# Optimization experiments

Hardware: AMD Instinct MI355X
Metric: run time of the kernel (lower is better)

## Reference

```python
import jax, jax.numpy as jnp
import numpy as np

DIM = 192
HEADS = 6
WH, WW = 8, 8
N = WH * WW
B_ = 2048
NW = 512


def _relative_position_index():
    coords = np.stack(np.meshgrid(np.arange(WH), np.arange(WW), indexing='ij'))  # 2,Wh,Ww
    cf = coords.reshape(2, -1)
    rel = cf[:, :, None] - cf[:, None, :]  # 2,N,N
    rel = rel.transpose(1, 2, 0).astype(np.int32)
    rel[:, :, 0] += WH - 1
    rel[:, :, 1] += WW - 1
    rel[:, :, 0] *= 2 * WW - 1
    return jnp.asarray(rel.sum(-1))  # N,N int32


def setup_inputs() -> dict:
    key = jax.random.key(0)
    ks = jax.random.split(key, 16)
    s = 0.02
    inp = {
        'q': jax.random.normal(ks[0], (B_, N, DIM), jnp.float32),
        'k': jax.random.normal(ks[1], (B_, N, DIM), jnp.float32),
        'v': jax.random.normal(ks[2], (B_, N, DIM), jnp.float32),
        'mask': jax.random.normal(ks[3], (NW, N, N), jnp.float32),
        'attn_mask': jax.random.randint(ks[4], (B_, 1, N, N), 0, 2).astype(bool),
        'Wq': jax.random.normal(ks[5], (DIM, DIM), jnp.float32) * s,
        'bq': jnp.zeros((DIM,), jnp.float32),
        'Wk': jax.random.normal(ks[6], (DIM, DIM), jnp.float32) * s,
        'bk': jnp.zeros((DIM,), jnp.float32),
        'Wv': jax.random.normal(ks[7], (DIM, DIM), jnp.float32) * s,
        'bv': jnp.zeros((DIM,), jnp.float32),
        'Wp': jax.random.normal(ks[8], (DIM, DIM), jnp.float32) * s,
        'bp': jnp.zeros((DIM,), jnp.float32),
        'rpb_table': jax.random.normal(ks[9], ((2 * WH - 1) * (2 * WW - 1), HEADS), jnp.float32) * s,
        'rel_idx': _relative_position_index(),
    }
    return inp


def reference(q, k, v, mask, attn_mask, Wq, bq, Wk, bk, Wv, bv, Wp, bp, rpb_table, rel_idx):
    Bw, n, C = q.shape
    hd = C // HEADS
    scale = hd ** (-0.5)
    # linear projections (torch Linear: x @ W.T + b), split heads -> b h n d
    qh = (q @ Wq.T + bq).reshape(Bw, n, HEADS, hd).transpose(0, 2, 1, 3) * scale
    kh = (k @ Wk.T + bk).reshape(Bw, n, HEADS, hd).transpose(0, 2, 1, 3)
    vh = (v @ Wv.T + bv).reshape(Bw, n, HEADS, hd).transpose(0, 2, 1, 3)
    attn = jnp.einsum('bhnd,bhmd->bhnm', qh, kh)  # (B_, H, N, N)
    attn = jnp.where(attn_mask, jnp.float32(-1e9), attn)
    # relative position bias gather: (N,N,H) -> (H,N,N)
    bias = rpb_table[rel_idx.reshape(-1)].reshape(n, n, HEADS).transpose(2, 0, 1)
    attn = attn + bias[None]
    nW = mask.shape[0]
    attn = attn.reshape(Bw // nW, nW, HEADS, n, n) + mask[None, :, None]
    attn = jax.nn.softmax(attn.reshape(Bw, HEADS, n, n), axis=-1)
    x = jnp.einsum('bhnm,bhmd->bhnd', attn, vh).transpose(0, 2, 1, 3).reshape(Bw, n, C)
    return x @ Wp.T + bp
```

## Files before the change

### kernel.cpp

```cpp
#include <hip/hip_runtime.h>

#define DIM    192
#define HEADS  6
#define HD     32
#define NTOK   64
#define NWIN   512
#define NBLK   2048
#define TPB    384
#define XPITCH 200
#define MPITCH 65

typedef short  bf16x4 __attribute__((ext_vector_type(4)));
typedef short  bf16x8 __attribute__((ext_vector_type(8)));
typedef float  f32x4  __attribute__((ext_vector_type(4)));

#if defined(__HIP_DEVICE_COMPILE__)
#if !__has_builtin(__builtin_amdgcn_mfma_f32_16x16x32_bf16)
#error "missing __builtin_amdgcn_mfma_f32_16x16x32_bf16"
#endif
#if !__has_builtin(__builtin_amdgcn_mfma_f32_16x16x16bf16_1k)
#error "missing __builtin_amdgcn_mfma_f32_16x16x16bf16_1k"
#endif
#endif

static __device__ __forceinline__ unsigned short f2bf(float f){
  unsigned u = __builtin_bit_cast(unsigned, f);
  u += 0x7FFFu + ((u >> 16) & 1u);
  return (unsigned short)(u >> 16);
}

static __device__ __forceinline__ f32x4 mfma32(bf16x8 a, bf16x8 b, f32x4 c){
  return __builtin_amdgcn_mfma_f32_16x16x32_bf16(a, b, c, 0, 0, 0);
}
static __device__ __forceinline__ f32x4 mfma16(bf16x4 a, bf16x4 b, f32x4 c){
  return __builtin_amdgcn_mfma_f32_16x16x16bf16_1k(a, b, c, 0, 0, 0);
}

static __device__ __forceinline__ bf16x8 load_wfrag(const float* __restrict__ W, int row, int k0){
  const float4 a = *(const float4*)(W + row*DIM + k0);
  const float4 b = *(const float4*)(W + row*DIM + k0 + 4);
  bf16x8 r;
  r[0]=(short)f2bf(a.x); r[1]=(short)f2bf(a.y); r[2]=(short)f2bf(a.z); r[3]=(short)f2bf(a.w);
  r[4]=(short)f2bf(b.x); r[5]=(short)f2bf(b.y); r[6]=(short)f2bf(b.z); r[7]=(short)f2bf(b.w);
  return r;
}

static __device__ __forceinline__ void stage_xin(unsigned short* xin, const float* __restrict__ src, int t){
  #pragma unroll
  for (int j = 0; j < 8; ++j){
    const int i4  = t + j*TPB;
    const float4 f = ((const float4*)src)[i4];
    const int row = i4 / 48;
    const int col = (i4 - row*48) * 4;
    uint2 u;
    u.x = (unsigned)f2bf(f.x) | ((unsigned)f2bf(f.y) << 16);
    u.y = (unsigned)f2bf(f.z) | ((unsigned)f2bf(f.w) << 16);
    *(uint2*)(xin + row*XPITCH + col) = u;
  }
}

__global__ void detect_amask_kernel(const unsigned int* __restrict__ am, int* __restrict__ mode){
  __shared__ int sawFloat, sawByte;
  if (threadIdx.x == 0){ sawFloat = 0; sawByte = 0; }
  __syncthreads();
  const uint4 ld = ((const uint4*)am)[threadIdx.x];
  unsigned w[4] = {ld.x, ld.y, ld.z, ld.w};
  int f = 0, bm = 0;
  #pragma unroll
  for (int i = 0; i < 4; ++i){
    if (w[i] == 0x3F800000u) f = 1;
    else if (w[i] & ~1u)     bm = 1;
  }
  if (f)  atomicOr(&sawFloat, 1);
  if (bm) atomicOr(&sawByte, 1);
  __syncthreads();
  if (threadIdx.x == 0) *mode = sawFloat ? 2 : (sawByte ? 1 : 0);
}

__global__ void bias_pre_kernel(const float* __restrict__ rpb, const int* __restrict__ rel_idx,
                                float* __restrict__ bias_pre){
  const int e = blockIdx.x*256 + threadIdx.x;
  if (e >= HEADS*NTOK*NTOK) return;
  const int rest = e & 4095, m = rest >> 6, n = rest & 63;
  bias_pre[e] = rpb[rel_idx[n*NTOK + m]*HEADS + (e >> 12)];
}

__global__ __launch_bounds__(TPB, 2) void swin_kernel(
  const float* __restrict__ q, const float* __restrict__ kin, const float* __restrict__ vin,
  const float* __restrict__ mask, const void* __restrict__ amask,
  const float* __restrict__ Wq, const float* __restrict__ bq,
  const float* __restrict__ Wk, const float* __restrict__ bk,
  const float* __restrict__ Wv, const float* __restrict__ bv,
  const float* __restrict__ Wp, const float* __restrict__ bp,
  const float* __restrict__ bias_pre, const int* __restrict__ mflag,
  float* __restrict__ out)
{
  __shared__ unsigned short xin[NTOK * XPITCH];
  __shared__ float madd[NTOK * MPITCH];

  const int b    = blockIdx.x;
  const int t    = threadIdx.x;
  const int h    = t >> 6;
  const int lane = t & 63;
  const int l15  = lane & 15;
  const int g    = lane >> 4;
  const int c0   = h * HD;
  const size_t base = (size_t)b * (NTOK * DIM);
  const float scale = 0.17677669529663687f;
  const f32x4 fz = {0.f, 0.f, 0.f, 0.f};

  {
    const int mode = mflag[0];
    const float* mrow = mask + (size_t)(b & (NWIN-1)) * (NTOK*NTOK);
    const size_t abase = (size_t)b * (NTOK*NTOK);
    for (int i = t; i < NTOK*NTOK; i += TPB){
      const int n = i >> 6, m = i & 63;
      bool msk;
      if (mode == 0)      msk = ((const int*)amask)[abase + i] != 0;
      else if (mode == 1) msk = ((const unsigned char*)amask)[abase + i] != 0;
      else                msk = ((const float*)amask)[abase + i] != 0.0f;
      madd[m*MPITCH + n] = mrow[i] + (msk ? -1e9f : 0.0f);
    }
    stage_xin(xin, q + base, t);
  }
  __syncthreads();

  bf16x4 Qf[4][2], Kf[4][2], Vf[2][4];

  {
    f32x4 acc[2][4];
    #pragma unroll
    for (int a0=0;a0<2;++a0){
      #pragma unroll
      for (int a1=0;a1<4;++a1) acc[a0][a1] = fz;
    }
    #pragma unroll
    for (int kt = 0; kt < 6; ++kt){
      const int k0 = kt*32 + g*8;
      const bf16x8 w0 = load_wfrag(Wq, c0 + l15, k0);
      const bf16x8 w1 = load_wfrag(Wq, c0 + 16 + l15, k0);
      #pragma unroll
      for (int nt = 0; nt < 4; ++nt){
        const bf16x8 xf = *(const bf16x8*)(xin + (nt*16 + l15)*XPITCH + k0);
        acc[0][nt] = mfma32(w0, xf, acc[0][nt]);
        acc[1][nt] = mfma32(w1, xf, acc[1][nt]);
      }
    }
    #pragma unroll
    for (int dt = 0; dt < 2; ++dt){
      const float4 bb = *(const float4*)(bq + c0 + dt*16 + g*4);
      #pragma unroll
      for (int nt = 0; nt < 4; ++nt){
        bf16x4 f;
        f[0]=(short)f2bf((acc[dt][nt][0]+bb.x)*scale);
        f[1]=(short)f2bf((acc[dt][nt][1]+bb.y)*scale);
        f[2]=(short)f2bf((acc[dt][nt][2]+bb.z)*scale);
        f[3]=(short)f2bf((acc[dt][nt][3]+bb.w)*scale);
        Qf[nt][dt] = f;
      }
    }
  }
  __syncthreads();
  stage_xin(xin, kin + base, t);
  __syncthreads();

  {
    f32x4 acc[2][4];
    #pragma unroll
    for (int a0=0;a0<2;++a0){
      #pragma unroll
      for (int a1=0;a1<4;++a1) acc[a0][a1] = fz;
    }
    #pragma unroll
    for (int kt = 0; kt < 6; ++kt){
      const int k0 = kt*32 + g*8;
      const bf16x8 w0 = load_wfrag(Wk, c0 + l15, k0);
      const bf16x8 w1 = load_wfrag(Wk, c0 + 16 + l15, k0);
      #pragma unroll
      for (int mt = 0; mt < 4; ++mt){
        const bf16x8 xf = *(const bf16x8*)(xin + (mt*16 + l15)*XPITCH + k0);
        acc[0][mt] = mfma32(w0, xf, acc[0][mt]);
        acc[1][mt] = mfma32(w1, xf, acc[1][mt]);
      }
    }
    #pragma unroll
    for (int dt = 0; dt < 2; ++dt){
      const float4 bb = *(const float4*)(bk + c0 + dt*16 + g*4);
      #pragma unroll
      for (int mt = 0; mt < 4; ++mt){
        bf16x4 f;
        f[0]=(short)f2bf(acc[dt][mt][0]+bb.x);
        f[1]=(short)f2bf(acc[dt][mt][1]+bb.y);
        f[2]=(short)f2bf(acc[dt][mt][2]+bb.z);
        f[3]=(short)f2bf(acc[dt][mt][3]+bb.w);
        Kf[mt][dt] = f;
      }
    }
  }
  __syncthreads();
  stage_xin(xin, vin + base, t);
  __syncthreads();

  {
    f32x4 acc[4][2];
    #pragma unroll
    for (int a0=0;a0<4;++a0){
      #pragma unroll
      for (int a1=0;a1<2;++a1) acc[a0][a1] = fz;
    }
    #pragma unroll
    for (int kt = 0; kt < 6; ++kt){
      const int k0 = kt*32 + g*8;
      const bf16x8 w0 = load_wfrag(Wv, c0 + l15, k0);
      const bf16x8 w1 = load_wfrag(Wv, c0 + 16 + l15, k0);
      #pragma unroll
      for (int mt = 0; mt < 4; ++mt){
        const bf16x8 xf = *(const bf16x8*)(xin + (mt*16 + l15)*XPITCH + k0);
        acc[mt][0] = mfma32(xf, w0, acc[mt][0]);
        acc[mt][1] = mfma32(xf, w1, acc[mt][1]);
      }
    }
    const float bv0 = bv[c0 + l15];
    const float bv1 = bv[c0 + 16 + l15];
    #pragma unroll
    for (int mt = 0; mt < 4; ++mt){
      bf16x4 f0, f1;
      f0[0]=(short)f2bf(acc[mt][0][0]+bv0); f0[1]=(short)f2bf(acc[mt][0][1]+bv0);
      f0[2]=(short)f2bf(acc[mt][0][2]+bv0); f0[3]=(short)f2bf(acc[mt][0][3]+bv0);
      f1[0]=(short)f2bf(acc[mt][1][0]+bv1); f1[1]=(short)f2bf(acc[mt][1][1]+bv1);
      f1[2]=(short)f2bf(acc[mt][1][2]+bv1); f1[3]=(short)f2bf(acc[mt][1][3]+bv1);
      Vf[0][mt] = f0;
      Vf[1][mt] = f1;
    }
  }
  __syncthreads();

  f32x4 s[4][4];
  #pragma unroll
  for (int mt = 0; mt < 4; ++mt){
    #pragma unroll
    for (int nt = 0; nt < 4; ++nt){
      f32x4 a = mfma16(Kf[mt][0], Qf[nt][0], fz);
      s[mt][nt] = mfma16(Kf[mt][1], Qf[nt][1], a);
    }
  }

  const float* bh = bias_pre + h * (NTOK*NTOK);
  bf16x4 Pf[4][4];
  #pragma unroll
  for (int nt = 0; nt < 4; ++nt){
    const int n = nt*16 + l15;
    float mx = -3.0e38f;
    #pragma unroll
    for (int mt = 0; mt < 4; ++mt){
      #pragma unroll
      for (int r = 0; r < 4; ++r){
        const int m = mt*16 + g*4 + r;
        const float val = s[mt][nt][r] + madd[m*MPITCH + n] + bh[m*64 + n];
        s[mt][nt][r] = val;
        mx = fmaxf(mx, val);
      }
    }
    mx = fmaxf(mx, __shfl_xor(mx, 16, 64));
    mx = fmaxf(mx, __shfl_xor(mx, 32, 64));
    float sum = 0.f;
    #pragma unroll
    for (int mt = 0; mt < 4; ++mt){
      #pragma unroll
      for (int r = 0; r < 4; ++r){
        const float e = __expf(s[mt][nt][r] - mx);
        s[mt][nt][r] = e;
        sum += e;
      }
    }
    sum += __shfl_xor(sum, 16, 64);
    sum += __shfl_xor(sum, 32, 64);
    const float inv = 1.0f / sum;
    #pragma unroll
    for (int ms = 0; ms < 4; ++ms){
      bf16x4 f;
      f[0]=(short)f2bf(s[ms][nt][0]*inv); f[1]=(short)f2bf(s[ms][nt][1]*inv);
      f[2]=(short)f2bf(s[ms][nt][2]*inv); f[3]=(short)f2bf(s[ms][nt][3]*inv);
      Pf[nt][ms] = f;
    }
  }

  f32x4 o[2][4];
  #pragma unroll
  for (int a0=0;a0<2;++a0){
    #pragma unroll
    for (int a1=0;a1<4;++a1) o[a0][a1] = fz;
  }
  #pragma unroll
  for (int ms = 0; ms < 4; ++ms){
    #pragma unroll
    for (int dt = 0; dt < 2; ++dt){
      #pragma unroll
      for (int nt = 0; nt < 4; ++nt){
        o[dt][nt] = mfma16(Vf[dt][ms], Pf[nt][ms], o[dt][nt]);
      }
    }
  }

  #pragma unroll
  for (int dt = 0; dt < 2; ++dt){
    #pragma unroll
    for (int nt = 0; nt < 4; ++nt){
      const int n   = nt*16 + l15;
      const int col = c0 + dt*16 + g*4;
      uint2 u;
      u.x = (unsigned)f2bf(o[dt][nt][0]) | ((unsigned)f2bf(o[dt][nt][1]) << 16);
      u.y = (unsigned)f2bf(o[dt][nt][2]) | ((unsigned)f2bf(o[dt][nt][3]) << 16);
      *(uint2*)(xin + n*XPITCH + col) = u;
    }
  }
  __syncthreads();

  {
    f32x4 acc[4][2];
    #pragma unroll
    for (int a0=0;a0<4;++a0){
      #pragma unroll
      for (int a1=0;a1<2;++a1) acc[a0][a1] = fz;
    }
    #pragma unroll
    for (int kt = 0; kt < 6; ++kt){
      const int k0 = kt*32 + g*8;
      const bf16x8 w0 = load_wfrag(Wp, c0 + l15, k0);
      const bf16x8 w1 = load_wfrag(Wp, c0 + 16 + l15, k0);
      #pragma unroll
      for (int nt = 0; nt < 4; ++nt){
        const bf16x8 xf = *(const bf16x8*)(xin + (nt*16 + l15)*XPITCH + k0);
        acc[nt][0] = mfma32(xf, w0, acc[nt][0]);
        acc[nt][1] = mfma32(xf, w1, acc[nt][1]);
      }
    }
    const float bp0 = bp[c0 + l15];
    const float bp1 = bp[c0 + 16 + l15];
    #pragma unroll
    for (int nt = 0; nt < 4; ++nt){
      #pragma unroll
      for (int ctl = 0; ctl < 2; ++ctl){
        const int c = c0 + ctl*16 + l15;
        const float badd = ctl ? bp1 : bp0;
        #pragma unroll
        for (int r = 0; r < 4; ++r){
          const int n = nt*16 + g*4 + r;
          out[base + (size_t)(n*DIM + c)] = acc[nt][ctl][r] + badd;
        }
      }
    }
  }
}

extern "C" void kernel_launch(void* const* d_in, const int* in_sizes, int n_in,
                              void* d_out, int out_size, void* d_ws, size_t ws_size,
                              hipStream_t stream){
  const float* q     = (const float*)d_in[0];
  const float* k     = (const float*)d_in[1];
  const float* v     = (const float*)d_in[2];
  const float* mask  = (const float*)d_in[3];
  const void*  amask = d_in[4];
  const float* Wq    = (const float*)d_in[5];
  const float* bq    = (const float*)d_in[6];
  const float* Wk    = (const float*)d_in[7];
  const float* bk    = (const float*)d_in[8];
  const float* Wv    = (const float*)d_in[9];
  const float* bv    = (const float*)d_in[10];
  const float* Wp    = (const float*)d_in[11];
  const float* bp    = (const float*)d_in[12];
  const float* rpb   = (const float*)d_in[13];
  const int*   ridx  = (const int*)d_in[14];
  float* out = (float*)d_out;
  float* bias_pre = (float*)d_ws;
  int*   mflag    = (int*)((char*)d_ws + 98304);

  detect_amask_kernel<<<1, 256, 0, stream>>>((const unsigned int*)amask, mflag);
  bias_pre_kernel<<<96, 256, 0, stream>>>(rpb, ridx, bias_pre);
  swin_kernel<<<NBLK, TPB, 0, stream>>>(q, k, v, mask, amask,
                                        Wq, bq, Wk, bk, Wv, bv, Wp, bp,
                                        bias_pre, mflag, out);
}
```

Before: 408.4 us.

## Pre-convert weights to bf16, double-buffer Q/K staging, prefetch V into registers

Adds a small kernel that converts the four weight matrices to bf16 once per call, so every block loads bf16 fragments directly instead of converting fp32 per block. Q and K are staged together into two LDS buffers, which removes a barrier pair between projections. V rows are prefetched into registers before the Q/K projections so the global load latency overlaps with compute. Launch bounds are raised to three blocks per CU. The trade-offs are more LDS per block, more registers for the prefetch, and an extra small kernel launch.

```diff
diff --git a/kernel.cpp b/kernel.cpp
--- a/kernel.cpp
+++ b/kernel.cpp
@@ -9,6 +9,7 @@
 #define TPB    384
 #define XPITCH 200
 #define MPITCH 65
+#define WMAT   (DIM*DIM)
 
 typedef short  bf16x4 __attribute__((ext_vector_type(4)));
 typedef short  bf16x8 __attribute__((ext_vector_type(8)));
@@ -36,26 +37,25 @@
   return __builtin_amdgcn_mfma_f32_16x16x16bf16_1k(a, b, c, 0, 0, 0);
 }
 
-static __device__ __forceinline__ bf16x8 load_wfrag(const float* __restrict__ W, int row, int k0){
-  const float4 a = *(const float4*)(W + row*DIM + k0);
-  const float4 b = *(const float4*)(W + row*DIM + k0 + 4);
-  bf16x8 r;
-  r[0]=(short)f2bf(a.x); r[1]=(short)f2bf(a.y); r[2]=(short)f2bf(a.z); r[3]=(short)f2bf(a.w);
-  r[4]=(short)f2bf(b.x); r[5]=(short)f2bf(b.y); r[6]=(short)f2bf(b.z); r[7]=(short)f2bf(b.w);
-  return r;
-}
-
-static __device__ __forceinline__ void stage_xin(unsigned short* xin, const float* __restrict__ src, int t){
+static __device__ __forceinline__ bf16x8 wfrag(const unsigned short* __restrict__ W, int row, int k0){
+  return *(const bf16x8*)(W + row*DIM + k0);
+}
+
+static __device__ __forceinline__ uint2 pack_bf(const float4 f){
+  uint2 u;
+  u.x = (unsigned)f2bf(f.x) | ((unsigned)f2bf(f.y) << 16);
+  u.y = (unsigned)f2bf(f.z) | ((unsigned)f2bf(f.w) << 16);
+  return u;
+}
+
+static __device__ __forceinline__ void stage_xin(unsigned short* xt, const float* __restrict__ src, int t){
   #pragma unroll
   for (int j = 0; j < 8; ++j){
     const int i4  = t + j*TPB;
     const float4 f = ((const float4*)src)[i4];
     const int row = i4 / 48;
     const int col = (i4 - row*48) * 4;
-    uint2 u;
-    u.x = (unsigned)f2bf(f.x) | ((unsigned)f2bf(f.y) << 16);
-    u.y = (unsigned)f2bf(f.z) | ((unsigned)f2bf(f.w) << 16);
-    *(uint2*)(xin + row*XPITCH + col) = u;
+    *(uint2*)(xt + row*XPITCH + col) = pack_bf(f);
   }
 }
 
@@ -85,17 +85,30 @@
   bias_pre[e] = rpb[rel_idx[n*NTOK + m]*HEADS + (e >> 12)];
 }
 
-__global__ __launch_bounds__(TPB, 2) void swin_kernel(
+__global__ void wconv_kernel(const float* __restrict__ Wq, const float* __restrict__ Wk,
+                             const float* __restrict__ Wv, const float* __restrict__ Wp,
+                             unsigned short* __restrict__ wbf){
+  const int e4 = blockIdx.x*256 + threadIdx.x;
+  if (e4 >= 4*WMAT/4) return;
+  const int mat = e4 / (WMAT/4);
+  const int off = e4 - mat*(WMAT/4);
+  const float* src = (mat==0)?Wq:(mat==1)?Wk:(mat==2)?Wv:Wp;
+  const float4 f = ((const float4*)src)[off];
+  unsigned short* dst = wbf + mat*WMAT + off*4;
+  dst[0]=f2bf(f.x); dst[1]=f2bf(f.y); dst[2]=f2bf(f.z); dst[3]=f2bf(f.w);
+}
+
+__global__ __launch_bounds__(TPB, 3) void swin_kernel(
   const float* __restrict__ q, const float* __restrict__ kin, const float* __restrict__ vin,
   const float* __restrict__ mask, const void* __restrict__ amask,
-  const float* __restrict__ Wq, const float* __restrict__ bq,
-  const float* __restrict__ Wk, const float* __restrict__ bk,
-  const float* __restrict__ Wv, const float* __restrict__ bv,
-  const float* __restrict__ Wp, const float* __restrict__ bp,
+  const unsigned short* __restrict__ wbf,
+  const float* __restrict__ bq, const float* __restrict__ bk,
+  const float* __restrict__ bv, const float* __restrict__ bp,
   const float* __restrict__ bias_pre, const int* __restrict__ mflag,
   float* __restrict__ out)
 {
-  __shared__ unsigned short xin[NTOK * XPITCH];
+  __shared__ unsigned short xa[NTOK * XPITCH];
+  __shared__ unsigned short xb[NTOK * XPITCH];
   __shared__ float madd[NTOK * MPITCH];
 
   const int b    = blockIdx.x;
@@ -108,6 +121,11 @@
   const size_t base = (size_t)b * (NTOK * DIM);
   const float scale = 0.17677669529663687f;
   const f32x4 fz = {0.f, 0.f, 0.f, 0.f};
+
+  const unsigned short* Wq = wbf;
+  const unsigned short* Wk = wbf + WMAT;
+  const unsigned short* Wv = wbf + 2*WMAT;
+  const unsigned short* Wp = wbf + 3*WMAT;
 
   {
     const int mode = mflag[0];
@@ -121,11 +139,16 @@
       else                msk = ((const float*)amask)[abase + i] != 0.0f;
       madd[m*MPITCH + n] = mrow[i] + (msk ? -1e9f : 0.0f);
     }
-    stage_xin(xin, q + base, t);
+    stage_xin(xa, q + base, t);
+    stage_xin(xb, kin + base, t);
   }
   __syncthreads();
 
   bf16x4 Qf[4][2], Kf[4][2], Vf[2][4];
+
+  float4 vpre[8];
+  #pragma unroll
+  for (int j = 0; j < 8; ++j) vpre[j] = ((const float4*)(vin + base))[t + j*TPB];
 
   {
     f32x4 acc[2][4];
@@ -137,11 +160,11 @@
     #pragma unroll
     for (int kt = 0; kt < 6; ++kt){
       const int k0 = kt*32 + g*8;
-      const bf16x8 w0 = load_wfrag(Wq, c0 + l15, k0);
-      const bf16x8 w1 = load_wfrag(Wq, c0 + 16 + l15, k0);
+      const bf16x8 w0 = wfrag(Wq, c0 + l15, k0);
+      const bf16x8 w1 = wfrag(Wq, c0 + 16 + l15, k0);
       #pragma unroll
       for (int nt = 0; nt < 4; ++nt){
-        const bf16x8 xf = *(const bf16x8*)(xin + (nt*16 + l15)*XPITCH + k0);
+        const bf16x8 xf = *(const bf16x8*)(xa + (nt*16 + l15)*XPITCH + k0);
         acc[0][nt] = mfma32(w0, xf, acc[0][nt]);
         acc[1][nt] = mfma32(w1, xf, acc[1][nt]);
       }
@@ -160,10 +183,6 @@
       }
     }
   }
-  __syncthreads();
-  stage_xin(xin, kin + base, t);
-  __syncthreads();
-
   {
     f32x4 acc[2][4];
     #pragma unroll
@@ -174,11 +193,11 @@
     #pragma unroll
     for (int kt = 0; kt < 6; ++kt){
       const int k0 = kt*32 + g*8;
-      const bf16x8 w0 = load_wfrag(Wk, c0 + l15, k0);
-      const bf16x8 w1 = load_wfrag(Wk, c0 + 16 + l15, k0);
+      const bf16x8 w0 = wfrag(Wk, c0 + l15, k0);
+      const bf16x8 w1 = wfrag(Wk, c0 + 16 + l15, k0);
       #pragma unroll
       for (int mt = 0; mt < 4; ++mt){
-        const bf16x8 xf = *(const bf16x8*)(xin + (mt*16 + l15)*XPITCH + k0);
+        const bf16x8 xf = *(const bf16x8*)(xb + (mt*16 + l15)*XPITCH + k0);
         acc[0][mt] = mfma32(w0, xf, acc[0][mt]);
         acc[1][mt] = mfma32(w1, xf, acc[1][mt]);
       }
@@ -198,7 +217,14 @@
     }
   }
   __syncthreads();
-  stage_xin(xin, vin + base, t);
+
+  #pragma unroll
+  for (int j = 0; j < 8; ++j){
+    const int i4  = t + j*TPB;
+    const int row = i4 / 48;
+    const int col = (i4 - row*48) * 4;
+    *(uint2*)(xa + row*XPITCH + col) = pack_bf(vpre[j]);
+  }
   __syncthreads();
 
   {
@@ -211,11 +237,11 @@
     #pragma unroll
     for (int kt = 0; kt < 6; ++kt){
       const int k0 = kt*32 + g*8;
-      const bf16x8 w0 = load_wfrag(Wv, c0 + l15, k0);
-      const bf16x8 w1 = load_wfrag(Wv, c0 + 16 + l15, k0);
+      const bf16x8 w0 = wfrag(Wv, c0 + l15, k0);
+      const bf16x8 w1 = wfrag(Wv, c0 + 16 + l15, k0);
       #pragma unroll
       for (int mt = 0; mt < 4; ++mt){
-        const bf16x8 xf = *(const bf16x8*)(xin + (mt*16 + l15)*XPITCH + k0);
+        const bf16x8 xf = *(const bf16x8*)(xa + (mt*16 + l15)*XPITCH + k0);
         acc[mt][0] = mfma32(xf, w0, acc[mt][0]);
         acc[mt][1] = mfma32(xf, w1, acc[mt][1]);
       }
@@ -233,7 +259,6 @@
       Vf[1][mt] = f1;
     }
   }
-  __syncthreads();
 
   f32x4 s[4][4];
   #pragma unroll
@@ -311,7 +336,7 @@
       uint2 u;
       u.x = (unsigned)f2bf(o[dt][nt][0]) | ((unsigned)f2bf(o[dt][nt][1]) << 16);
       u.y = (unsigned)f2bf(o[dt][nt][2]) | ((unsigned)f2bf(o[dt][nt][3]) << 16);
-      *(uint2*)(xin + n*XPITCH + col) = u;
+      *(uint2*)(xb + n*XPITCH + col) = u;
     }
   }
   __syncthreads();
@@ -326,11 +351,11 @@
     #pragma unroll
     for (int kt = 0; kt < 6; ++kt){
       const int k0 = kt*32 + g*8;
-      const bf16x8 w0 = load_wfrag(Wp, c0 + l15, k0);
-      const bf16x8 w1 = load_wfrag(Wp, c0 + 16 + l15, k0);
+      const bf16x8 w0 = wfrag(Wp, c0 + l15, k0);
+      const bf16x8 w1 = wfrag(Wp, c0 + 16 + l15, k0);
       #pragma unroll
       for (int nt = 0; nt < 4; ++nt){
-        const bf16x8 xf = *(const bf16x8*)(xin + (nt*16 + l15)*XPITCH + k0);
+        const bf16x8 xf = *(const bf16x8*)(xb + (nt*16 + l15)*XPITCH + k0);
         acc[nt][0] = mfma32(xf, w0, acc[nt][0]);
         acc[nt][1] = mfma32(xf, w1, acc[nt][1]);
       }
@@ -372,12 +397,15 @@
   const float* rpb   = (const float*)d_in[13];
   const int*   ridx  = (const int*)d_in[14];
   float* out = (float*)d_out;
-  float* bias_pre = (float*)d_ws;
-  int*   mflag    = (int*)((char*)d_ws + 98304);
+
+  float*          bias_pre = (float*)d_ws;
+  int*            mflag    = (int*)((char*)d_ws + 98304);
+  unsigned short* wbf      = (unsigned short*)((char*)d_ws + 98560);
 
   detect_amask_kernel<<<1, 256, 0, stream>>>((const unsigned int*)amask, mflag);
   bias_pre_kernel<<<96, 256, 0, stream>>>(rpb, ridx, bias_pre);
-  swin_kernel<<<NBLK, TPB, 0, stream>>>(q, k, v, mask, amask,
-                                        Wq, bq, Wk, bk, Wv, bv, Wp, bp,
+  wconv_kernel<<<144, 256, 0, stream>>>(Wq, Wk, Wv, Wp, wbf);
+  swin_kernel<<<NBLK, TPB, 0, stream>>>(q, k, v, mask, amask, wbf,
+                                        bq, bk, bv, bp,
                                         bias_pre, mflag, out);
 }
```

Result: faster. 378.0 us (-7.4%).
